# Kernel optimization log

Measured on AMD Instinct MI355X. Metric: run time of the kernel, lower is better.

Reference implementation:

```python
import jax, jax.numpy as jnp
import numpy as np

N, DIN, DOUT = 8192, 2048, 2048


def setup_inputs() -> dict:
    key = jax.random.key(0)
    k1, k2, k3 = jax.random.split(key, 3)
    x = jax.random.normal(k1, (N, DIN), dtype=jnp.float32)
    # quantized params: uint8 kernel, uint16 bias (as produced by model.quantize)
    qkernel = jax.random.randint(k2, (DIN, DOUT), 0, 256, dtype=jnp.int32).astype(jnp.uint8)
    qbias = jax.random.randint(k3, (DOUT,), 0, 65536, dtype=jnp.int32).astype(jnp.uint16)
    scale = jnp.array(0.5, dtype=jnp.float32)
    zero_point = jnp.array(0.5, dtype=jnp.float32)
    return {"x": x, "scale": scale, "zero_point": zero_point,
            "qkernel": qkernel, "qbias": qbias}


def reference(x, scale, zero_point, qkernel, qbias) -> jnp.ndarray:
    # quantize(x, b=8, uint8): clip(round(x/scale) + zero_point, 0, 255)
    qmax = 2 ** 8 - 1
    xq = jnp.clip(jnp.round(x / scale) + zero_point, 0, qmax).astype(jnp.uint8)
    acc = jnp.dot(xq, qkernel, preferred_element_type=jnp.uint16)
    acc = (acc + qbias).astype(jnp.uint32)  # uint16 add wraps, then widen
    # dequantize: (x - zero_point) * scale  -> float32
    return (acc - zero_point) * scale
```

## Files before the change

### kernel.cpp

```cpp
#include <hip/hip_runtime.h>
#include <stdint.h>


#define NROWS 8192
#define DIN   2048
#define DOUT  2048

typedef int v4i __attribute__((ext_vector_type(4)));

__device__ inline void gload16(const uint8_t* g, uint8_t* l) {
  __builtin_amdgcn_global_load_lds(
      (__attribute__((address_space(1))) void*)(g),
      (__attribute__((address_space(3))) void*)(l), 16, 0, 0);
}

__device__ inline void wgbar() {
  __builtin_amdgcn_sched_barrier(0);
  __builtin_amdgcn_s_barrier();
  __builtin_amdgcn_sched_barrier(0);
}

__device__ inline uint32_t q4(float4 v, float inv, float z, int& sum) {
  uint32_t w = 0;
  float e[4] = {v.x, v.y, v.z, v.w};
#pragma unroll
  for (int i = 0; i < 4; ++i) {
    float tq = rintf(e[i] * inv) + z;
    tq = fminf(fmaxf(tq, 0.0f), 255.0f);
    uint32_t q = (uint32_t)tq;
    sum += (int)q;
    w |= ((q ^ 0x80u) & 0xFFu) << (8 * i);
  }
  return w;
}

__global__ __launch_bounds__(256) void kp(const float* __restrict__ x,
                                          const float* __restrict__ sp,
                                          const float* __restrict__ zpp,
                                          const void* __restrict__ qk,
                                          const void* __restrict__ qbias,
                                          uint8_t* __restrict__ xq,
                                          int* __restrict__ rs128,
                                          uint8_t* __restrict__ qkT,
                                          int* __restrict__ qb32) {
  const int t = threadIdx.x;
  if (blockIdx.x < NROWS) {
    const int row = blockIdx.x;
    const float s = sp[0], z = zpp[0];
    const float inv = 1.0f / s;
    const float4* xr = (const float4*)(x + (size_t)row * DIN);
    float4 a = xr[t];
    float4 b = xr[t + 256];
    int sum = 0;
    uint32_t w0 = q4(a, inv, z, sum);
    uint32_t w1 = q4(b, inv, z, sum);
    uint32_t* xw = (uint32_t*)(xq + (size_t)row * DIN);
    xw[t] = w0;
    xw[t + 256] = w1;
#pragma unroll
    for (int o = 32; o > 0; o >>= 1) sum += __shfl_down(sum, o);
    __shared__ int ws4[4];
    if ((t & 63) == 0) ws4[t >> 6] = sum;
    __syncthreads();
    if (t == 0) rs128[row] = 128 * (ws4[0] + ws4[1] + ws4[2] + ws4[3]);
    return;
  }
  __shared__ uint8_t tile[64][68];
  __shared__ int sflag;
  if (t == 0) sflag = 0;
  __syncthreads();
  {
    const int* q32 = (const int*)qk;
    int bad = 0;
#pragma unroll
    for (int i = 0; i < 4; ++i) bad |= ((unsigned)q32[t + 256 * i] > 255u);
    if (bad) sflag = 1;
  }
  __syncthreads();
  const int u8mode = sflag;

  const int j = blockIdx.x - NROWS;
  const int n0 = (j & 31) * 64;
  const int k0 = (j >> 5) * 64;
  const int tx = t & 15;
  const int ty = t >> 4;
  if (u8mode) {
    const uint8_t* q8 = (const uint8_t*)qk;
#pragma unroll
    for (int jj = 0; jj < 4; ++jj) {
      int r = jj * 16 + ty;
      uint32_t w = *(const uint32_t*)(q8 + (size_t)(k0 + r) * DOUT + n0 + tx * 4);
      tile[r][tx * 4 + 0] = (uint8_t)(w & 255u);
      tile[r][tx * 4 + 1] = (uint8_t)((w >> 8) & 255u);
      tile[r][tx * 4 + 2] = (uint8_t)((w >> 16) & 255u);
      tile[r][tx * 4 + 3] = (uint8_t)((w >> 24) & 255u);
    }
  } else {
    const int* q32 = (const int*)qk;
#pragma unroll
    for (int jj = 0; jj < 4; ++jj) {
      int r = jj * 16 + ty;
      int4 w = *(const int4*)(q32 + (size_t)(k0 + r) * DOUT + n0 + tx * 4);
      tile[r][tx * 4 + 0] = (uint8_t)w.x;
      tile[r][tx * 4 + 1] = (uint8_t)w.y;
      tile[r][tx * 4 + 2] = (uint8_t)w.z;
      tile[r][tx * 4 + 3] = (uint8_t)w.w;
    }
  }
  __syncthreads();
#pragma unroll
  for (int jj = 0; jj < 4; ++jj) {
    int r = jj * 16 + ty;
    uint32_t b0 = tile[tx * 4 + 0][r];
    uint32_t b1 = tile[tx * 4 + 1][r];
    uint32_t b2 = tile[tx * 4 + 2][r];
    uint32_t b3 = tile[tx * 4 + 3][r];
    *(uint32_t*)(qkT + (size_t)(n0 + r) * DIN + k0 + tx * 4) =
        (b0 ^ 0x80u) | ((b1 ^ 0x80u) << 8) | ((b2 ^ 0x80u) << 16) | ((b3 ^ 0x80u) << 24);
  }
  if (k0 == 0 && t < 64) {
    int n = n0 + t;
    qb32[n] = u8mode ? (int)((const uint16_t*)qbias)[n] : ((const int*)qbias)[n];
  }
}

__global__ __launch_bounds__(512, 2) void kg(const uint8_t* __restrict__ A,
                                             const uint8_t* __restrict__ B,
                                             const int* __restrict__ rs128,
                                             const int* __restrict__ qb32,
                                             const float* __restrict__ sp,
                                             const float* __restrict__ zpp,
                                             float* __restrict__ out) {
  __shared__ __align__(16) uint8_t lds[131072];
  const int t = threadIdx.x;
  const int l = t & 63, wid = t >> 6;
  const int wr = wid >> 2, wc = wid & 3;
  const int rl = l & 15, kgp = l >> 4;

  const int bid = blockIdx.x;
  const int swz = (bid & 7) * 32 + (bid >> 3);
  const int m0 = (swz >> 3) * 256;
  const int n0 = (swz & 7) * 256;

  const int srow = t >> 2;
  const int sc = (t & 3) ^ ((srow >> 1) & 3);
  const uint8_t* gA = A + (size_t)(m0 + srow) * DIN + sc * 16;
  const uint8_t* gA2 = gA + (size_t)128 * DIN;
  const uint8_t* gB = B + (size_t)(n0 + srow) * DIN + sc * 16;
  const uint8_t* gB2 = gB + (size_t)128 * DIN;
  const int sdst = t * 16;

#define STAGE_A(BUF, KS, KB) do {                                   \
    uint8_t* d_ = lds + (BUF) * 32768 + (KS) * 16384 + sdst;        \
    gload16(gA + (KB) + (KS) * 64, d_);                             \
    gload16(gA2 + (KB) + (KS) * 64, d_ + 8192);                     \
  } while (0)
#define STAGE_B(BUF, KS, KB) do {                                   \
    uint8_t* d_ = lds + 65536 + (BUF) * 32768 + (KS) * 16384 + sdst;\
    gload16(gB + (KB) + (KS) * 64, d_);                             \
    gload16(gB2 + (KB) + (KS) * 64, d_ + 8192);                     \
  } while (0)

  const int swl = (rl >> 1) & 3;
  const int aoff0 = (wr * 128 + rl) * 64 + ((kgp ^ swl) << 4);
  const int boff0 = 65536 + (wc * 64 + rl) * 64 + ((kgp ^ swl) << 4);

  v4i acc[8][4];
#pragma unroll
  for (int i = 0; i < 8; ++i)
#pragma unroll
    for (int j = 0; j < 4; ++j) acc[i][j] = (v4i){0, 0, 0, 0};
  v4i csum[4];
#pragma unroll
  for (int j = 0; j < 4; ++j) csum[j] = (v4i){0, 0, 0, 0};
  const v4i ones = (v4i){0x01010101, 0x01010101, 0x01010101, 0x01010101};
  v4i af[4], bf[4];

#define LD_A(BUF, MH, KH) do {                                       \
    const uint8_t* ap_ = lds + (BUF) * 32768 + (KH) * 16384 + aoff0 + (MH) * 4096; \
    _Pragma("unroll")                                                \
    for (int q = 0; q < 4; ++q) af[q] = *(const v4i*)(ap_ + q * 1024);\
  } while (0)
#define LD_B(BUF, KH) do {                                           \
    const uint8_t* bp_ = lds + (BUF) * 32768 + (KH) * 16384 + boff0; \
    _Pragma("unroll")                                                \
    for (int nj = 0; nj < 4; ++nj) bf[nj] = *(const v4i*)(bp_ + nj * 1024); \
  } while (0)
#define CLUSTER(MH, CS) do {                                         \
    _Pragma("unroll")                                                \
    for (int q = 0; q < 4; ++q)                                      \
      _Pragma("unroll")                                              \
      for (int nj = 0; nj < 4; ++nj)                                 \
        acc[(MH) * 4 + q][nj] = __builtin_amdgcn_mfma_i32_16x16x64_i8(\
            af[q], bf[nj], acc[(MH) * 4 + q][nj], 0, 0, 0);          \
    if (CS) {                                                        \
      _Pragma("unroll")                                              \
      for (int nj = 0; nj < 4; ++nj)                                 \
        csum[nj] = __builtin_amdgcn_mfma_i32_16x16x64_i8(            \
            ones, bf[nj], csum[nj], 0, 0, 0);                        \
    }                                                                \
  } while (0)

  STAGE_A(0, 0, 0);
  STAGE_B(0, 0, 0);
  STAGE_A(0, 1, 0);
  STAGE_B(0, 1, 0);
  STAGE_A(1, 0, 128);
  STAGE_B(1, 0, 128);
  STAGE_A(1, 1, 128);
  STAGE_B(1, 1, 128);
  asm volatile("s_waitcnt vmcnt(8)" ::: "memory");
  wgbar();

  for (int tt = 0; tt < 16; ++tt) {
    const int cur = tt & 1;
    LD_B(cur, 0);
    LD_A(cur, 0, 0);
    CLUSTER(0, 1);
    LD_A(cur, 1, 0);
    CLUSTER(1, 0);
    LD_B(cur, 1);
    LD_A(cur, 0, 1);
    CLUSTER(0, 1);
    LD_A(cur, 1, 1);
    CLUSTER(1, 0);
    asm volatile("s_waitcnt vmcnt(0)" ::: "memory");
    wgbar();
    if (tt < 14) {
      const int kn = (tt + 2) * 128;
      STAGE_A(cur, 0, kn);
      STAGE_B(cur, 0, kn);
      STAGE_A(cur, 1, kn);
      STAGE_B(cur, 1, kn);
    }
  }

  const float s = sp[0], z = zpp[0];
  int cc[4];
#pragma unroll
  for (int nj = 0; nj < 4; ++nj) cc[nj] = (csum[nj][0] << 7) + qb32[n0 + wc * 64 + nj * 16 + rl];
#pragma unroll
  for (int mi = 0; mi < 8; ++mi) {
#pragma unroll
    for (int r = 0; r < 4; ++r) {
      int row = m0 + wr * 128 + mi * 16 + kgp * 4 + r;
      int rs = rs128[row];
#pragma unroll
      for (int nj = 0; nj < 4; ++nj) {
        int col = n0 + wc * 64 + nj * 16 + rl;
        uint32_t v = (uint32_t)(acc[mi][nj][r] + rs + cc[nj]) & 0xFFFFu;
        out[(size_t)row * DOUT + col] = ((float)v - z) * s;
      }
    }
  }
#undef STAGE_A
#undef STAGE_B
#undef LD_A
#undef LD_B
#undef CLUSTER
}

extern "C" void kernel_launch(void* const* d_in, const int* in_sizes, int n_in,
                              void* d_out, int out_size, void* d_ws, size_t ws_size,
                              hipStream_t stream) {
  const float* x   = (const float*)d_in[0];
  const float* sp  = (const float*)d_in[1];
  const float* zpp = (const float*)d_in[2];
  const void*  qk  = d_in[3];
  const void*  qb  = d_in[4];
  float* out = (float*)d_out;

  uint8_t* ws = (uint8_t*)d_ws;
  uint8_t* xq  = ws;
  uint8_t* qkT = ws + (16u << 20);
  int* rs128 = (int*)(ws + (20u << 20));
  int* qb32  = (int*)(ws + (20u << 20) + (32u << 10));

  kp<<<NROWS + (DIN / 64) * (DOUT / 64), 256, 0, stream>>>(
      x, sp, zpp, qk, qb, xq, rs128, qkT, qb32);
  kg<<<dim3(256), 512, 0, stream>>>(xq, qkT, rs128, qb32, sp, zpp, out);
}
```

Baseline: 166.0 us.

## Shrink GEMM tile to 128x256 with triple-buffered k64 stages and precomputed column sums

The GEMM tile drops from 256x256 to 128x256 and the grid grows to 512 blocks. The k-loop now uses 64-wide stages in a 3-deep LDS ring, which cuts LDS use and raises the occupancy target, and the next stage is prefetched before the MFMAs, which run at raised priority. The per-column weight sums were computed with extra ones-MFMAs inside the GEMM; they now come from 8 extra prep blocks that scan the kernel column-wise and fold in the bias. The cost is less A/B reuse per tile, and those prep blocks run long serial loops over the columns.

New measurement: 215.5 us. 1.3x slower.

```diff
diff --git a/kernel.cpp b/kernel.cpp
--- a/kernel.cpp
+++ b/kernel.cpp
@@ -32,6 +32,13 @@
     w |= ((q ^ 0x80u) & 0xFFu) << (8 * i);
   }
   return w;
+}
+
+__device__ inline int qk_is_u8(const int* q32, int t) {
+  int bad = 0;
+#pragma unroll
+  for (int i = 0; i < 4; ++i) bad |= ((unsigned)q32[t + 256 * i] > 255u);
+  return bad;
 }
 
 __global__ __launch_bounds__(256) void kp(const float* __restrict__ x,
@@ -42,7 +49,7 @@
                                           uint8_t* __restrict__ xq,
                                           int* __restrict__ rs128,
                                           uint8_t* __restrict__ qkT,
-                                          int* __restrict__ qb32) {
+                                          int* __restrict__ ccomb) {
   const int t = threadIdx.x;
   if (blockIdx.x < NROWS) {
     const int row = blockIdx.x;
@@ -65,20 +72,31 @@
     if (t == 0) rs128[row] = 128 * (ws4[0] + ws4[1] + ws4[2] + ws4[3]);
     return;
   }
-  __shared__ uint8_t tile[64][68];
   __shared__ int sflag;
   if (t == 0) sflag = 0;
   __syncthreads();
-  {
-    const int* q32 = (const int*)qk;
-    int bad = 0;
-#pragma unroll
-    for (int i = 0; i < 4; ++i) bad |= ((unsigned)q32[t + 256 * i] > 255u);
-    if (bad) sflag = 1;
-  }
+  if (qk_is_u8((const int*)qk, t)) sflag = 1;
   __syncthreads();
   const int u8mode = sflag;
 
+  if (blockIdx.x >= NROWS + (DIN / 64) * (DOUT / 64)) {
+    const int n = (blockIdx.x - NROWS - (DIN / 64) * (DOUT / 64)) * 256 + t;
+    int sum = 0;
+    if (u8mode) {
+      const uint8_t* q8 = (const uint8_t*)qk;
+#pragma unroll 8
+      for (int k = 0; k < DIN; ++k) sum += (int)q8[(size_t)k * DOUT + n];
+    } else {
+      const int* q32 = (const int*)qk;
+#pragma unroll 8
+      for (int k = 0; k < DIN; ++k) sum += q32[(size_t)k * DOUT + n];
+    }
+    int qb = u8mode ? (int)((const uint16_t*)qbias)[n] : ((const int*)qbias)[n];
+    ccomb[n] = (sum << 7) + qb;
+    return;
+  }
+
+  __shared__ uint8_t tile[64][68];
   const int j = blockIdx.x - NROWS;
   const int n0 = (j & 31) * 64;
   const int k0 = (j >> 5) * 64;
@@ -118,146 +136,97 @@
     *(uint32_t*)(qkT + (size_t)(n0 + r) * DIN + k0 + tx * 4) =
         (b0 ^ 0x80u) | ((b1 ^ 0x80u) << 8) | ((b2 ^ 0x80u) << 16) | ((b3 ^ 0x80u) << 24);
   }
-  if (k0 == 0 && t < 64) {
-    int n = n0 + t;
-    qb32[n] = u8mode ? (int)((const uint16_t*)qbias)[n] : ((const int*)qbias)[n];
-  }
-}
-
-__global__ __launch_bounds__(512, 2) void kg(const uint8_t* __restrict__ A,
+}
+
+__global__ __launch_bounds__(512, 4) void kg(const uint8_t* __restrict__ A,
                                              const uint8_t* __restrict__ B,
                                              const int* __restrict__ rs128,
-                                             const int* __restrict__ qb32,
+                                             const int* __restrict__ ccomb,
                                              const float* __restrict__ sp,
                                              const float* __restrict__ zpp,
                                              float* __restrict__ out) {
-  __shared__ __align__(16) uint8_t lds[131072];
+  __shared__ __align__(16) uint8_t lds[3 * 24576];
   const int t = threadIdx.x;
   const int l = t & 63, wid = t >> 6;
   const int wr = wid >> 2, wc = wid & 3;
   const int rl = l & 15, kgp = l >> 4;
 
   const int bid = blockIdx.x;
-  const int swz = (bid & 7) * 32 + (bid >> 3);
-  const int m0 = (swz >> 3) * 256;
-  const int n0 = (swz & 7) * 256;
+  const int m0 = (bid >> 3) * 128;
+  const int n0 = (bid & 7) * 256;
 
   const int srow = t >> 2;
   const int sc = (t & 3) ^ ((srow >> 1) & 3);
   const uint8_t* gA = A + (size_t)(m0 + srow) * DIN + sc * 16;
-  const uint8_t* gA2 = gA + (size_t)128 * DIN;
   const uint8_t* gB = B + (size_t)(n0 + srow) * DIN + sc * 16;
   const uint8_t* gB2 = gB + (size_t)128 * DIN;
   const int sdst = t * 16;
 
-#define STAGE_A(BUF, KS, KB) do {                                   \
-    uint8_t* d_ = lds + (BUF) * 32768 + (KS) * 16384 + sdst;        \
-    gload16(gA + (KB) + (KS) * 64, d_);                             \
-    gload16(gA2 + (KB) + (KS) * 64, d_ + 8192);                     \
+#define STAGE(SB, KB) do {                                           \
+    uint8_t* d_ = lds + (SB) * 24576 + sdst;                         \
+    gload16(gA + (KB), d_);                                          \
+    gload16(gB + (KB), d_ + 8192);                                   \
+    gload16(gB2 + (KB), d_ + 16384);                                 \
   } while (0)
-#define STAGE_B(BUF, KS, KB) do {                                   \
-    uint8_t* d_ = lds + 65536 + (BUF) * 32768 + (KS) * 16384 + sdst;\
-    gload16(gB + (KB) + (KS) * 64, d_);                             \
-    gload16(gB2 + (KB) + (KS) * 64, d_ + 8192);                     \
-  } while (0)
 
   const int swl = (rl >> 1) & 3;
-  const int aoff0 = (wr * 128 + rl) * 64 + ((kgp ^ swl) << 4);
-  const int boff0 = 65536 + (wc * 64 + rl) * 64 + ((kgp ^ swl) << 4);
-
-  v4i acc[8][4];
-#pragma unroll
-  for (int i = 0; i < 8; ++i)
+  const int aoff = (wr * 64 + rl) * 64 + ((kgp ^ swl) << 4);
+  const int boff = 8192 + (wc * 64 + rl) * 64 + ((kgp ^ swl) << 4);
+
+  v4i acc[4][4];
+#pragma unroll
+  for (int i = 0; i < 4; ++i)
 #pragma unroll
     for (int j = 0; j < 4; ++j) acc[i][j] = (v4i){0, 0, 0, 0};
-  v4i csum[4];
-#pragma unroll
-  for (int j = 0; j < 4; ++j) csum[j] = (v4i){0, 0, 0, 0};
-  const v4i ones = (v4i){0x01010101, 0x01010101, 0x01010101, 0x01010101};
-  v4i af[4], bf[4];
-
-#define LD_A(BUF, MH, KH) do {                                       \
-    const uint8_t* ap_ = lds + (BUF) * 32768 + (KH) * 16384 + aoff0 + (MH) * 4096; \
-    _Pragma("unroll")                                                \
-    for (int q = 0; q < 4; ++q) af[q] = *(const v4i*)(ap_ + q * 1024);\
-  } while (0)
-#define LD_B(BUF, KH) do {                                           \
-    const uint8_t* bp_ = lds + (BUF) * 32768 + (KH) * 16384 + boff0; \
-    _Pragma("unroll")                                                \
-    for (int nj = 0; nj < 4; ++nj) bf[nj] = *(const v4i*)(bp_ + nj * 1024); \
-  } while (0)
-#define CLUSTER(MH, CS) do {                                         \
-    _Pragma("unroll")                                                \
-    for (int q = 0; q < 4; ++q)                                      \
-      _Pragma("unroll")                                              \
-      for (int nj = 0; nj < 4; ++nj)                                 \
-        acc[(MH) * 4 + q][nj] = __builtin_amdgcn_mfma_i32_16x16x64_i8(\
-            af[q], bf[nj], acc[(MH) * 4 + q][nj], 0, 0, 0);          \
-    if (CS) {                                                        \
-      _Pragma("unroll")                                              \
-      for (int nj = 0; nj < 4; ++nj)                                 \
-        csum[nj] = __builtin_amdgcn_mfma_i32_16x16x64_i8(            \
-            ones, bf[nj], csum[nj], 0, 0, 0);                        \
-    }                                                                \
-  } while (0)
-
-  STAGE_A(0, 0, 0);
-  STAGE_B(0, 0, 0);
-  STAGE_A(0, 1, 0);
-  STAGE_B(0, 1, 0);
-  STAGE_A(1, 0, 128);
-  STAGE_B(1, 0, 128);
-  STAGE_A(1, 1, 128);
-  STAGE_B(1, 1, 128);
-  asm volatile("s_waitcnt vmcnt(8)" ::: "memory");
+
+  STAGE(0, 0);
+  STAGE(1, 64);
+  asm volatile("s_waitcnt vmcnt(3)" ::: "memory");
   wgbar();
 
-  for (int tt = 0; tt < 16; ++tt) {
-    const int cur = tt & 1;
-    LD_B(cur, 0);
-    LD_A(cur, 0, 0);
-    CLUSTER(0, 1);
-    LD_A(cur, 1, 0);
-    CLUSTER(1, 0);
-    LD_B(cur, 1);
-    LD_A(cur, 0, 1);
-    CLUSTER(0, 1);
-    LD_A(cur, 1, 1);
-    CLUSTER(1, 0);
-    asm volatile("s_waitcnt vmcnt(0)" ::: "memory");
+  int rb = 0, sb = 2;
+  for (int tt = 0; tt < 32; ++tt) {
+    const uint8_t* base = lds + rb * 24576;
+    v4i af[4], bf[4];
+#pragma unroll
+    for (int mi = 0; mi < 4; ++mi) af[mi] = *(const v4i*)(base + aoff + mi * 1024);
+#pragma unroll
+    for (int nj = 0; nj < 4; ++nj) bf[nj] = *(const v4i*)(base + boff + nj * 1024);
+    STAGE(sb, ((tt + 2) & 31) * 64);
+    __builtin_amdgcn_s_setprio(1);
+#pragma unroll
+    for (int mi = 0; mi < 4; ++mi)
+#pragma unroll
+      for (int nj = 0; nj < 4; ++nj)
+        acc[mi][nj] = __builtin_amdgcn_mfma_i32_16x16x64_i8(af[mi], bf[nj], acc[mi][nj], 0, 0, 0);
+    __builtin_amdgcn_s_setprio(0);
+    asm volatile("s_waitcnt vmcnt(3)" ::: "memory");
     wgbar();
-    if (tt < 14) {
-      const int kn = (tt + 2) * 128;
-      STAGE_A(cur, 0, kn);
-      STAGE_B(cur, 0, kn);
-      STAGE_A(cur, 1, kn);
-      STAGE_B(cur, 1, kn);
-    }
+    rb = (rb == 2) ? 0 : rb + 1;
+    sb = (sb == 2) ? 0 : sb + 1;
   }
 
   const float s = sp[0], z = zpp[0];
-  int cc[4];
-#pragma unroll
-  for (int nj = 0; nj < 4; ++nj) cc[nj] = (csum[nj][0] << 7) + qb32[n0 + wc * 64 + nj * 16 + rl];
-#pragma unroll
-  for (int mi = 0; mi < 8; ++mi) {
+  int cc[4], col[4];
+#pragma unroll
+  for (int nj = 0; nj < 4; ++nj) {
+    col[nj] = n0 + wc * 64 + nj * 16 + rl;
+    cc[nj] = ccomb[col[nj]];
+  }
+#pragma unroll
+  for (int mi = 0; mi < 4; ++mi) {
 #pragma unroll
     for (int r = 0; r < 4; ++r) {
-      int row = m0 + wr * 128 + mi * 16 + kgp * 4 + r;
+      int row = m0 + wr * 64 + mi * 16 + kgp * 4 + r;
       int rs = rs128[row];
 #pragma unroll
       for (int nj = 0; nj < 4; ++nj) {
-        int col = n0 + wc * 64 + nj * 16 + rl;
         uint32_t v = (uint32_t)(acc[mi][nj][r] + rs + cc[nj]) & 0xFFFFu;
-        out[(size_t)row * DOUT + col] = ((float)v - z) * s;
+        out[(size_t)row * DOUT + col[nj]] = ((float)v - z) * s;
       }
     }
   }
-#undef STAGE_A
-#undef STAGE_B
-#undef LD_A
-#undef LD_B
-#undef CLUSTER
+#undef STAGE
 }
 
 extern "C" void kernel_launch(void* const* d_in, const int* in_sizes, int n_in,
@@ -274,9 +243,9 @@
   uint8_t* xq  = ws;
   uint8_t* qkT = ws + (16u << 20);
   int* rs128 = (int*)(ws + (20u << 20));
-  int* qb32  = (int*)(ws + (20u << 20) + (32u << 10));
-
-  kp<<<NROWS + (DIN / 64) * (DOUT / 64), 256, 0, stream>>>(
-      x, sp, zpp, qk, qb, xq, rs128, qkT, qb32);
-  kg<<<dim3(256), 512, 0, stream>>>(xq, qkT, rs128, qb32, sp, zpp, out);
-}
+  int* ccomb = (int*)(ws + (20u << 20) + (32u << 10));
+
+  kp<<<NROWS + (DIN / 64) * (DOUT / 64) + 8, 256, 0, stream>>>(
+      x, sp, zpp, qk, qb, xq, rs128, qkT, ccomb);
+  kg<<<dim3(512), 512, 0, stream>>>(xq, qkT, rs128, ccomb, sp, zpp, out);
+}
```
